# Optimization experiments

Hardware: AMD Instinct MI355X
Metric: run time of the kernel (lower is better)

## Reference

```python
import jax, jax.numpy as jnp
import numpy as np

TOP_K = 2


def setup_inputs() -> dict:
    key = jax.random.key(0)
    k1, k2, k3, k4, k5 = jax.random.split(key, 5)
    B, S, D, E, F = 2, 1024, 2048, 8, 768
    scale_in = 1.0 / np.sqrt(D)
    scale_ff = 1.0 / np.sqrt(F)
    return {
        "x": jax.random.normal(k1, (B, S, D), dtype=jnp.float32),
        "w_gate_router": jax.random.normal(k2, (E, D), dtype=jnp.float32) * scale_in,
        "w_gate_proj": jax.random.normal(k3, (E, F, D), dtype=jnp.float32) * scale_in,
        "w_up_proj": jax.random.normal(k4, (E, F, D), dtype=jnp.float32) * scale_in,
        "w_down_proj": jax.random.normal(k5, (E, D, F), dtype=jnp.float32) * scale_ff,
    }


def moe_forward(x, w_gate_router, w_gate_proj, w_up_proj, w_down_proj):
    E = w_gate_router.shape[0]
    # Router: scores [B,S,E], top-k selection, softmax over the k selected scores.
    scores = jnp.einsum("bsd,ed->bse", x, w_gate_router)
    topk_scores, topk_idx = jax.lax.top_k(scores, TOP_K)          # [B,S,K]
    topk_probs = jax.nn.softmax(topk_scores, axis=-1)             # [B,S,K]
    # Dense combine weights: zero for unselected experts (== scatter of topk_probs).
    weights = jnp.sum(topk_probs[..., None] * jax.nn.one_hot(topk_idx, E, dtype=x.dtype), axis=-2)  # [B,S,E]
    # Per-expert SwiGLU computed densely over all tokens (same math as
    # gather/dispatch-per-expert followed by scatter-add combine).
    gate = jnp.einsum("bsd,efd->bsef", x, w_gate_proj)            # [B,S,E,F]
    up = jnp.einsum("bsd,efd->bsef", x, w_up_proj)
    hidden = jax.nn.silu(gate) * up                                # [B,S,E,F]
    # Weighted combine: sum_e weights[b,s,e] * (hidden @ w_down[e].T)
    out = jnp.einsum("bsef,edf,bse->bsd", hidden, w_down_proj, weights)
    return out


def reference(x, w_gate_router, w_gate_proj, w_up_proj, w_down_proj):
    return moe_forward(x, w_gate_router, w_gate_proj, w_up_proj, w_down_proj)
```

## Files before the change

kernel.cpp:

```cpp
#include <hip/hip_runtime.h>

#define T_TOK 2048
#define DIM   2048
#define NEXP  8
#define FF    768
#define NGRP  16
#define BK    32

typedef unsigned short u16;
typedef unsigned int   u32;
typedef __bf16 bf16x8 __attribute__((ext_vector_type(8)));
typedef float  f32x4  __attribute__((ext_vector_type(4)));
typedef u16    u16x4  __attribute__((ext_vector_type(4)));
typedef u16    u16x8  __attribute__((ext_vector_type(8)));

#define AS1 __attribute__((address_space(1)))
#define AS3 __attribute__((address_space(3)))

__device__ __forceinline__ u16 f2bf(float f) {
    union { u32 i; float f; } v; v.f = f;
    u32 r = v.i + 0x7FFF + ((v.i >> 16) & 1);
    return (u16)(r >> 16);
}
__device__ __forceinline__ float bf2f(u16 u) {
    union { u32 i; float f; } v; v.i = ((u32)u) << 16; return v.f;
}

__device__ __forceinline__ void gload16(const u16* g, u16* l) {
    __builtin_amdgcn_global_load_lds((const AS1 u32*)g, (AS3 u32*)l, 16, 0, 0);
}

__global__ void cvt3_kernel(const float* __restrict__ s0, u16* __restrict__ d0,
                            const float* __restrict__ s1, u16* __restrict__ d1,
                            const float* __restrict__ s2, u16* __restrict__ d2) {
    const float* __restrict__ s; u16* __restrict__ d;
    switch (blockIdx.y) {
        case 0: s = s0; d = d0; break;
        case 1: s = s1; d = d1; break;
        default: s = s2; d = d2; break;
    }
    const size_t st = 1536u * 256u;
    size_t t = (size_t)blockIdx.x * 256 + threadIdx.x;
#pragma unroll
    for (int it = 0; it < 4; it++) {
        size_t i = t + (size_t)it * st;
        f32x4 a = ((const f32x4*)s)[i * 2];
        f32x4 b = ((const f32x4*)s)[i * 2 + 1];
        u16x8 o;
#pragma unroll
        for (int j = 0; j < 4; j++) { o[j] = f2bf(a[j]); o[4 + j] = f2bf(b[j]); }
        ((u16x8*)d)[i] = o;
    }
}

__global__ void router_kernel(const float* __restrict__ x, const float* __restrict__ wr,
                              int* cnt, int* rt_e, float* rt_p, u16* __restrict__ xb) {
    int wave = threadIdx.x >> 6, lane = threadIdx.x & 63;
    int t = blockIdx.x * 4 + wave;
    float xv[32];
#pragma unroll
    for (int i = 0; i < 32; i++) xv[i] = x[(size_t)t * DIM + i * 64 + lane];
#pragma unroll
    for (int i = 0; i < 32; i++) xb[(size_t)t * DIM + i * 64 + lane] = f2bf(xv[i]);
    float s[NEXP];
#pragma unroll
    for (int e = 0; e < NEXP; e++) {
        float acc = 0.f;
#pragma unroll
        for (int i = 0; i < 32; i++) acc += xv[i] * wr[(size_t)e * DIM + i * 64 + lane];
        for (int off = 32; off; off >>= 1) acc += __shfl_xor(acc, off);
        s[e] = acc;
    }
    if (lane == 0) {
        int bi = 0; float bv = s[0];
        for (int e = 1; e < NEXP; e++) if (s[e] > bv) { bv = s[e]; bi = e; }
        float sv = -1e30f; int si = 0;
        for (int e = 0; e < NEXP; e++) { if (e == bi) continue; if (s[e] > sv) { sv = s[e]; si = e; } }
        float p0 = 1.f / (1.f + __expf(sv - bv));
        float p1 = 1.f - p0;
        rt_e[t * 2 + 0] = bi; rt_e[t * 2 + 1] = si;
        rt_p[t * 2 + 0] = p0; rt_p[t * 2 + 1] = p1;
        atomicAdd(&cnt[bi * 2 + 0], 1);
        atomicAdd(&cnt[si * 2 + 1], 1);
    }
}

__global__ void scanassign_kernel(const int* cnt, const int* rt_e, const float* rt_p,
                                  int* base_g, int* tile_g, int* tile_m0, int* ntiles,
                                  int* rowtok, float* rowprob) {
    __shared__ int s_base[NGRP];
    __shared__ int s_pos[NGRP];
    int tid = threadIdx.x;
    if (tid < NGRP) s_pos[tid] = 0;
    if (tid < 64) {
        int lane = tid;
        int c = (lane < NGRP) ? cnt[lane] : 0;
        int nt_g = (c + 127) >> 7;
        int pre = 0, tpre = 0;
        for (int i = 0; i < NGRP; i++) {
            int ci = __shfl(c, i), ti = __shfl(nt_g, i);
            if (i < lane) { pre += ci; tpre += ti; }
        }
        if (lane < NGRP) {
            s_base[lane] = pre; base_g[lane] = pre;
            for (int j = 0; j < nt_g; j++) { tile_g[tpre + j] = lane; tile_m0[tpre + j] = j * 128; }
            if (lane == NGRP - 1) *ntiles = tpre + nt_g;
        }
    }
    __syncthreads();
    for (int t = tid; t < T_TOK; t += 256) {
#pragma unroll
        for (int k = 0; k < 2; k++) {
            int g = rt_e[t * 2 + k] * 2 + k;
            int pos = atomicAdd(&s_pos[g], 1);
            int row = s_base[g] + pos;
            rowtok[row] = t;
            rowprob[row] = rt_p[t * 2 + k];
        }
    }
}

__launch_bounds__(256)
__global__ void gateup_kernel(const u16* __restrict__ xb, const u16* __restrict__ wgb,
                              const u16* __restrict__ wub,
                              const int* cnt, const int* base, const int* tile_g,
                              const int* tile_m0, const int* ntiles,
                              const int* rowtok, const float* rowprob,
                              u16* __restrict__ hidden) {
    int tile = blockIdx.x;
    if (tile >= *ntiles) return;
    int g = tile_g[tile], m0 = tile_m0[tile];
    int e = g >> 1;
    int f0 = blockIdx.y * 32;
    int cg = cnt[g], bg_ = base[g];

    __shared__ u16 As[2][128 * BK];
    __shared__ u16 Bs[2][64 * BK];
    __shared__ int   tks[128];
    __shared__ float ps[128];

    int tid = threadIdx.x;
    if (tid < 128) {
        int valid = (m0 + tid) < cg;
        tks[tid] = valid ? rowtok[bg_ + m0 + tid] : 0;
        ps[tid]  = valid ? rowprob[bg_ + m0 + tid] : 0.f;
    }
    __syncthreads();

    int wave = tid >> 6, lane = tid & 63;
    int quad = lane >> 4, l16 = lane & 15;
    int wr = wave >> 1, wc = wave & 1;

    int r4 = lane >> 2;
    int cw = ((lane & 3) ^ ((r4 >> 1) & 3)) * 8;

    const u16* gA0 = xb + (size_t)tks[wave * 32 + r4] * DIM + cw;
    const u16* gA1 = xb + (size_t)tks[wave * 32 + 16 + r4] * DIM + cw;
    int lA0 = (wave * 32) * BK, lA1 = (wave * 32 + 16) * BK;
    const u16* bsrc = (wave & 1) ? wub : wgb;
    const u16* gB = bsrc + ((size_t)e * FF + f0 + (wave >> 1) * 16 + r4) * DIM + cw;
    int lB = (wave * 16) * BK;

    int swz = (quad ^ ((l16 >> 1) & 3)) * 8;
    int aoff[4], boff[2];
#pragma unroll
    for (int mi = 0; mi < 4; mi++) aoff[mi] = (wr * 64 + mi * 16 + l16) * BK + swz;
#pragma unroll
    for (int ni = 0; ni < 2; ni++) boff[ni] = (wc * 32 + ni * 16 + l16) * BK + swz;

    f32x4 acc[4][2] = {};

    gload16(gA0, &As[0][0] + lA0);
    gload16(gA1, &As[0][0] + lA1);
    gload16(gB,  &Bs[0][0] + lB);

    for (int kt = 0; kt < DIM / BK; kt++) {
        int cur = kt & 1;
        int kk = (kt + 1) * BK;
        if (kk < DIM) {
            gload16(gA0 + kk, &As[cur ^ 1][0] + lA0);
            gload16(gA1 + kk, &As[cur ^ 1][0] + lA1);
            gload16(gB + kk,  &Bs[cur ^ 1][0] + lB);
            __builtin_amdgcn_sched_barrier(0);
            asm volatile("s_waitcnt vmcnt(3)" ::: "memory");
        } else {
            __builtin_amdgcn_sched_barrier(0);
            asm volatile("s_waitcnt vmcnt(0)" ::: "memory");
        }
        __builtin_amdgcn_s_barrier();
        __builtin_amdgcn_sched_barrier(0);
        bf16x8 a[4], b[2];
#pragma unroll
        for (int mi = 0; mi < 4; mi++) a[mi] = *(const bf16x8*)&As[cur][aoff[mi]];
#pragma unroll
        for (int ni = 0; ni < 2; ni++) b[ni] = *(const bf16x8*)&Bs[cur][boff[ni]];
#pragma unroll
        for (int mi = 0; mi < 4; mi++)
#pragma unroll
            for (int ni = 0; ni < 2; ni++)
                acc[mi][ni] = __builtin_amdgcn_mfma_f32_16x16x32_bf16(a[mi], b[ni], acc[mi][ni], 0, 0, 0);
        __builtin_amdgcn_sched_barrier(0);
        asm volatile("s_waitcnt lgkmcnt(0)" ::: "memory");
        __builtin_amdgcn_s_barrier();
    }

    int f = f0 + wc * 16 + l16;
#pragma unroll
    for (int mi = 0; mi < 4; mi++) {
#pragma unroll
        for (int r = 0; r < 4; r++) {
            int m = wr * 64 + mi * 16 + quad * 4 + r;
            if (m0 + m < cg) {
                float gv = acc[mi][0][r], uv = acc[mi][1][r];
                float h = (gv / (1.f + __expf(-gv))) * uv * ps[m];
                hidden[(size_t)(bg_ + m0 + m) * FF + f] = f2bf(h);
            }
        }
    }
}

__launch_bounds__(256)
__global__ void down_kernel(const u16* __restrict__ hid, const u16* __restrict__ wdb,
                            const int* cnt, const int* base, const int* tile_g,
                            const int* tile_m0, const int* ntiles, const int* rowtok,
                            u16* __restrict__ out0, u16* __restrict__ out1) {
    int tile = blockIdx.x;
    if (tile >= *ntiles) return;
    int g = tile_g[tile], m0 = tile_m0[tile];
    int e = g >> 1, slot = g & 1;
    int d0 = blockIdx.y * 64;
    int cg = cnt[g], bg_ = base[g];

    __shared__ u16 As[2][128 * BK];
    __shared__ u16 Bs[2][64 * BK];
    __shared__ int tks[128];

    int tid = threadIdx.x;
    if (tid < 128) tks[tid] = ((m0 + tid) < cg) ? rowtok[bg_ + m0 + tid] : 0;
    __syncthreads();

    int wave = tid >> 6, lane = tid & 63;
    int quad = lane >> 4, l16 = lane & 15;
    int wr = wave >> 1, wc = wave & 1;

    int r4 = lane >> 2;
    int cw = ((lane & 3) ^ ((r4 >> 1) & 3)) * 8;

    const u16* gA0 = hid + (size_t)(bg_ + m0 + wave * 32 + r4) * FF + cw;
    const u16* gA1 = hid + (size_t)(bg_ + m0 + wave * 32 + 16 + r4) * FF + cw;
    int lA0 = (wave * 32) * BK, lA1 = (wave * 32 + 16) * BK;
    const u16* gB = wdb + ((size_t)e * DIM + d0 + wave * 16 + r4) * FF + cw;
    int lB = (wave * 16) * BK;

    int swz = (quad ^ ((l16 >> 1) & 3)) * 8;
    int aoff[4], boff[2];
#pragma unroll
    for (int mi = 0; mi < 4; mi++) aoff[mi] = (wr * 64 + mi * 16 + l16) * BK + swz;
#pragma unroll
    for (int ni = 0; ni < 2; ni++) boff[ni] = (wc * 32 + ni * 16 + l16) * BK + swz;

    f32x4 acc[4][2] = {};

    gload16(gA0, &As[0][0] + lA0);
    gload16(gA1, &As[0][0] + lA1);
    gload16(gB,  &Bs[0][0] + lB);

    for (int kt = 0; kt < FF / BK; kt++) {
        int cur = kt & 1;
        int kk = (kt + 1) * BK;
        if (kk < FF) {
            gload16(gA0 + kk, &As[cur ^ 1][0] + lA0);
            gload16(gA1 + kk, &As[cur ^ 1][0] + lA1);
            gload16(gB + kk,  &Bs[cur ^ 1][0] + lB);
            __builtin_amdgcn_sched_barrier(0);
            asm volatile("s_waitcnt vmcnt(3)" ::: "memory");
        } else {
            __builtin_amdgcn_sched_barrier(0);
            asm volatile("s_waitcnt vmcnt(0)" ::: "memory");
        }
        __builtin_amdgcn_s_barrier();
        __builtin_amdgcn_sched_barrier(0);
        bf16x8 a[4], b[2];
#pragma unroll
        for (int mi = 0; mi < 4; mi++) a[mi] = *(const bf16x8*)&As[cur][aoff[mi]];
#pragma unroll
        for (int ni = 0; ni < 2; ni++) b[ni] = *(const bf16x8*)&Bs[cur][boff[ni]];
#pragma unroll
        for (int mi = 0; mi < 4; mi++)
#pragma unroll
            for (int ni = 0; ni < 2; ni++)
                acc[mi][ni] = __builtin_amdgcn_mfma_f32_16x16x32_bf16(a[mi], b[ni], acc[mi][ni], 0, 0, 0);
        __builtin_amdgcn_sched_barrier(0);
        asm volatile("s_waitcnt lgkmcnt(0)" ::: "memory");
        __builtin_amdgcn_s_barrier();
    }

    u16* outp = slot ? out1 : out0;
#pragma unroll
    for (int mi = 0; mi < 4; mi++) {
#pragma unroll
        for (int ni = 0; ni < 2; ni++) {
            int d = d0 + wc * 32 + ni * 16 + l16;
#pragma unroll
            for (int r = 0; r < 4; r++) {
                int m = wr * 64 + mi * 16 + quad * 4 + r;
                if (m0 + m < cg) {
                    outp[(size_t)tks[m] * DIM + d] = f2bf(acc[mi][ni][r]);
                }
            }
        }
    }
}

__global__ void combine_kernel(const u16* __restrict__ o0, const u16* __restrict__ o1,
                               float* __restrict__ out) {
    int i = blockIdx.x * blockDim.x + threadIdx.x;
    u16x8 a = *(const u16x8*)(o0 + (size_t)i * 8);
    u16x8 b = *(const u16x8*)(o1 + (size_t)i * 8);
    f32x4 r0, r1;
#pragma unroll
    for (int j = 0; j < 4; j++) {
        r0[j] = bf2f(a[j]) + bf2f(b[j]);
        r1[j] = bf2f(a[4 + j]) + bf2f(b[4 + j]);
    }
    *(f32x4*)(out + (size_t)i * 8) = r0;
    *(f32x4*)(out + (size_t)i * 8 + 4) = r1;
}

extern "C" void kernel_launch(void* const* d_in, const int* in_sizes, int n_in,
                              void* d_out, int out_size, void* d_ws, size_t ws_size,
                              hipStream_t stream) {
    const float* x  = (const float*)d_in[0];
    const float* wr = (const float*)d_in[1];
    const float* wg = (const float*)d_in[2];
    const float* wu = (const float*)d_in[3];
    const float* wd = (const float*)d_in[4];
    float* out = (float*)d_out;

    char* W = (char*)d_ws;
    int*   cnt     = (int*)(W + 0);
    int*   base    = (int*)(W + 128);
    int*   ntiles  = (int*)(W + 192);
    int*   tile_g  = (int*)(W + 256);
    int*   tile_m0 = (int*)(W + 512);
    int*   rt_e    = (int*)(W + 1024);
    float* rt_p    = (float*)(W + 20480);
    int*   rowtok  = (int*)(W + 40960);
    float* rowprob = (float*)(W + 61440);
    u16*   hidden  = (u16*)(W + 81920);
    u16*   xb      = (u16*)(W + ((size_t)8  << 20));
    u16*   wgb     = (u16*)(W + ((size_t)17 << 20));
    u16*   wub     = (u16*)(W + ((size_t)43 << 20));
    u16*   wdb     = (u16*)(W + ((size_t)69 << 20));
    u16*   out0    = (u16*)(W + ((size_t)17 << 20));
    u16*   out1    = (u16*)(W + ((size_t)26 << 20));

    hipMemsetAsync(W, 0, 256, stream);

    cvt3_kernel<<<dim3(1536, 3), 256, 0, stream>>>(wg, wgb, wu, wub, wd, wdb);

    router_kernel<<<T_TOK / 4, 256, 0, stream>>>(x, wr, cnt, rt_e, rt_p, xb);
    scanassign_kernel<<<1, 256, 0, stream>>>(cnt, rt_e, rt_p, base, tile_g, tile_m0,
                                             ntiles, rowtok, rowprob);

    gateup_kernel<<<dim3(48, 24), 256, 0, stream>>>(xb, wgb, wub, cnt, base, tile_g, tile_m0,
                                                    ntiles, rowtok, rowprob, hidden);
    down_kernel<<<dim3(48, 32), 256, 0, stream>>>(hidden, wdb, cnt, base, tile_g, tile_m0,
                                                  ntiles, rowtok, out0, out1);
    combine_kernel<<<T_TOK * DIM / (256 * 8), 256, 0, stream>>>(out0, out1, out);
}
```

Baseline: 381.2 us.

## Deepen gate-up and down GEMM pipelines to three LDS stages with BK=64

Both the grouped gate/up GEMM and the down GEMM now use a K tile of 64 instead of 32, with a triple-buffered LDS ring that keeps two tiles of global-to-LDS loads in flight. The XOR swizzle is reworked for 8-element column groups so the wider rows stay bank-conflict free. This halves the number of K iterations and their barriers and hides more load latency. In exchange LDS use per block roughly triples (about 72KB), which may cut occupancy, and the hard-coded vmcnt wait counts must match the number of loads issued per stage.

```diff
diff --git a/kernel.cpp b/kernel.cpp
--- a/kernel.cpp
+++ b/kernel.cpp
@@ -5,7 +5,7 @@
 #define NEXP  8
 #define FF    768
 #define NGRP  16
-#define BK    32
+#define BK    64
 
 typedef unsigned short u16;
 typedef unsigned int   u32;
@@ -134,8 +134,8 @@
     int f0 = blockIdx.y * 32;
     int cg = cnt[g], bg_ = base[g];
 
-    __shared__ u16 As[2][128 * BK];
-    __shared__ u16 Bs[2][64 * BK];
+    __shared__ u16 As[3][128 * BK];
+    __shared__ u16 Bs[3][64 * BK];
     __shared__ int   tks[128];
     __shared__ float ps[128];
 
@@ -151,58 +151,88 @@
     int quad = lane >> 4, l16 = lane & 15;
     int wr = wave >> 1, wc = wave & 1;
 
-    int r4 = lane >> 2;
-    int cw = ((lane & 3) ^ ((r4 >> 1) & 3)) * 8;
-
-    const u16* gA0 = xb + (size_t)tks[wave * 32 + r4] * DIM + cw;
-    const u16* gA1 = xb + (size_t)tks[wave * 32 + 16 + r4] * DIM + cw;
-    int lA0 = (wave * 32) * BK, lA1 = (wave * 32 + 16) * BK;
+    int r8  = lane >> 3;
+    int csw = ((lane & 7) ^ r8) * 8;
+
+    const u16* gA[4]; int lA[4];
+#pragma unroll
+    for (int gi = 0; gi < 4; gi++) {
+        int row = wave * 32 + gi * 8 + r8;
+        gA[gi] = xb + (size_t)tks[row] * DIM + csw;
+        lA[gi] = (wave * 32 + gi * 8) * BK;
+    }
     const u16* bsrc = (wave & 1) ? wub : wgb;
-    const u16* gB = bsrc + ((size_t)e * FF + f0 + (wave >> 1) * 16 + r4) * DIM + cw;
-    int lB = (wave * 16) * BK;
-
-    int swz = (quad ^ ((l16 >> 1) & 3)) * 8;
-    int aoff[4], boff[2];
-#pragma unroll
-    for (int mi = 0; mi < 4; mi++) aoff[mi] = (wr * 64 + mi * 16 + l16) * BK + swz;
-#pragma unroll
-    for (int ni = 0; ni < 2; ni++) boff[ni] = (wc * 32 + ni * 16 + l16) * BK + swz;
+    const u16* gB[2]; int lB[2];
+#pragma unroll
+    for (int gi = 0; gi < 2; gi++) {
+        int f = f0 + (wave >> 1) * 16 + gi * 8 + r8;
+        gB[gi] = bsrc + ((size_t)e * FF + f) * DIM + csw;
+        lB[gi] = (wave * 16 + gi * 8) * BK;
+    }
+
+    int sw0 = ((0 * 4 + quad) ^ (l16 & 7)) * 8;
+    int sw1 = ((1 * 4 + quad) ^ (l16 & 7)) * 8;
 
     f32x4 acc[4][2] = {};
 
-    gload16(gA0, &As[0][0] + lA0);
-    gload16(gA1, &As[0][0] + lA1);
-    gload16(gB,  &Bs[0][0] + lB);
-
-    for (int kt = 0; kt < DIM / BK; kt++) {
-        int cur = kt & 1;
-        int kk = (kt + 1) * BK;
-        if (kk < DIM) {
-            gload16(gA0 + kk, &As[cur ^ 1][0] + lA0);
-            gload16(gA1 + kk, &As[cur ^ 1][0] + lA1);
-            gload16(gB + kk,  &Bs[cur ^ 1][0] + lB);
-            __builtin_amdgcn_sched_barrier(0);
-            asm volatile("s_waitcnt vmcnt(3)" ::: "memory");
-        } else {
-            __builtin_amdgcn_sched_barrier(0);
-            asm volatile("s_waitcnt vmcnt(0)" ::: "memory");
-        }
+#define GU_STAGE(kkof, bi) do {                                          \
+    _Pragma("unroll")                                                    \
+    for (int gi = 0; gi < 4; gi++) gload16(gA[gi] + (kkof), &As[bi][0] + lA[gi]); \
+    _Pragma("unroll")                                                    \
+    for (int gi = 0; gi < 2; gi++) gload16(gB[gi] + (kkof), &Bs[bi][0] + lB[gi]); \
+} while (0)
+
+#define GU_COMPUTE(bi) do {                                              \
+    _Pragma("unroll")                                                    \
+    for (int ks = 0; ks < 2; ks++) {                                     \
+        int sw = ks ? sw1 : sw0;                                         \
+        bf16x8 a[4], b[2];                                               \
+        _Pragma("unroll")                                                \
+        for (int mi = 0; mi < 4; mi++)                                   \
+            a[mi] = *(const bf16x8*)&As[bi][(wr * 64 + mi * 16 + l16) * BK + sw]; \
+        _Pragma("unroll")                                                \
+        for (int ni = 0; ni < 2; ni++)                                   \
+            b[ni] = *(const bf16x8*)&Bs[bi][(wc * 32 + ni * 16 + l16) * BK + sw]; \
+        _Pragma("unroll")                                                \
+        for (int mi = 0; mi < 4; mi++)                                   \
+            _Pragma("unroll")                                            \
+            for (int ni = 0; ni < 2; ni++)                               \
+                acc[mi][ni] = __builtin_amdgcn_mfma_f32_16x16x32_bf16(a[mi], b[ni], acc[mi][ni], 0, 0, 0); \
+    }                                                                    \
+} while (0)
+
+    GU_STAGE(0, 0);
+    GU_STAGE(BK, 1);
+
+    const int NT = DIM / BK;
+    int cur = 0;
+    for (int kt = 0; kt < NT - 2; kt++) {
+        int s2 = cur + 2; if (s2 >= 3) s2 -= 3;
+        GU_STAGE((kt + 2) * BK, s2);
+        __builtin_amdgcn_sched_barrier(0);
+        asm volatile("s_waitcnt vmcnt(12)" ::: "memory");
         __builtin_amdgcn_s_barrier();
         __builtin_amdgcn_sched_barrier(0);
-        bf16x8 a[4], b[2];
-#pragma unroll
-        for (int mi = 0; mi < 4; mi++) a[mi] = *(const bf16x8*)&As[cur][aoff[mi]];
-#pragma unroll
-        for (int ni = 0; ni < 2; ni++) b[ni] = *(const bf16x8*)&Bs[cur][boff[ni]];
-#pragma unroll
-        for (int mi = 0; mi < 4; mi++)
-#pragma unroll
-            for (int ni = 0; ni < 2; ni++)
-                acc[mi][ni] = __builtin_amdgcn_mfma_f32_16x16x32_bf16(a[mi], b[ni], acc[mi][ni], 0, 0, 0);
+        GU_COMPUTE(cur);
         __builtin_amdgcn_sched_barrier(0);
         asm volatile("s_waitcnt lgkmcnt(0)" ::: "memory");
         __builtin_amdgcn_s_barrier();
-    }
+        cur++; if (cur >= 3) cur = 0;
+    }
+    __builtin_amdgcn_sched_barrier(0);
+    asm volatile("s_waitcnt vmcnt(6)" ::: "memory");
+    __builtin_amdgcn_s_barrier();
+    __builtin_amdgcn_sched_barrier(0);
+    GU_COMPUTE(cur);
+    cur++; if (cur >= 3) cur = 0;
+    __builtin_amdgcn_sched_barrier(0);
+    asm volatile("s_waitcnt vmcnt(0)" ::: "memory");
+    __builtin_amdgcn_s_barrier();
+    __builtin_amdgcn_sched_barrier(0);
+    GU_COMPUTE(cur);
+
+#undef GU_STAGE
+#undef GU_COMPUTE
 
     int f = f0 + wc * 16 + l16;
 #pragma unroll
@@ -231,8 +261,8 @@
     int d0 = blockIdx.y * 64;
     int cg = cnt[g], bg_ = base[g];
 
-    __shared__ u16 As[2][128 * BK];
-    __shared__ u16 Bs[2][64 * BK];
+    __shared__ u16 As[3][128 * BK];
+    __shared__ u16 Bs[3][64 * BK];
     __shared__ int tks[128];
 
     int tid = threadIdx.x;
@@ -243,57 +273,87 @@
     int quad = lane >> 4, l16 = lane & 15;
     int wr = wave >> 1, wc = wave & 1;
 
-    int r4 = lane >> 2;
-    int cw = ((lane & 3) ^ ((r4 >> 1) & 3)) * 8;
-
-    const u16* gA0 = hid + (size_t)(bg_ + m0 + wave * 32 + r4) * FF + cw;
-    const u16* gA1 = hid + (size_t)(bg_ + m0 + wave * 32 + 16 + r4) * FF + cw;
-    int lA0 = (wave * 32) * BK, lA1 = (wave * 32 + 16) * BK;
-    const u16* gB = wdb + ((size_t)e * DIM + d0 + wave * 16 + r4) * FF + cw;
-    int lB = (wave * 16) * BK;
-
-    int swz = (quad ^ ((l16 >> 1) & 3)) * 8;
-    int aoff[4], boff[2];
-#pragma unroll
-    for (int mi = 0; mi < 4; mi++) aoff[mi] = (wr * 64 + mi * 16 + l16) * BK + swz;
-#pragma unroll
-    for (int ni = 0; ni < 2; ni++) boff[ni] = (wc * 32 + ni * 16 + l16) * BK + swz;
+    int r8  = lane >> 3;
+    int csw = ((lane & 7) ^ r8) * 8;
+
+    const u16* gA[4]; int lA[4];
+#pragma unroll
+    for (int gi = 0; gi < 4; gi++) {
+        int row = wave * 32 + gi * 8 + r8;
+        gA[gi] = hid + (size_t)(bg_ + m0 + row) * FF + csw;
+        lA[gi] = (wave * 32 + gi * 8) * BK;
+    }
+    const u16* gB[2]; int lB[2];
+#pragma unroll
+    for (int gi = 0; gi < 2; gi++) {
+        int n = wave * 16 + gi * 8 + r8;
+        gB[gi] = wdb + ((size_t)e * DIM + d0 + n) * FF + csw;
+        lB[gi] = (wave * 16 + gi * 8) * BK;
+    }
+
+    int sw0 = ((0 * 4 + quad) ^ (l16 & 7)) * 8;
+    int sw1 = ((1 * 4 + quad) ^ (l16 & 7)) * 8;
 
     f32x4 acc[4][2] = {};
 
-    gload16(gA0, &As[0][0] + lA0);
-    gload16(gA1, &As[0][0] + lA1);
-    gload16(gB,  &Bs[0][0] + lB);
-
-    for (int kt = 0; kt < FF / BK; kt++) {
-        int cur = kt & 1;
-        int kk = (kt + 1) * BK;
-        if (kk < FF) {
-            gload16(gA0 + kk, &As[cur ^ 1][0] + lA0);
-            gload16(gA1 + kk, &As[cur ^ 1][0] + lA1);
-            gload16(gB + kk,  &Bs[cur ^ 1][0] + lB);
-            __builtin_amdgcn_sched_barrier(0);
-            asm volatile("s_waitcnt vmcnt(3)" ::: "memory");
-        } else {
-            __builtin_amdgcn_sched_barrier(0);
-            asm volatile("s_waitcnt vmcnt(0)" ::: "memory");
-        }
+#define DN_STAGE(kkof, bi) do {                                          \
+    _Pragma("unroll")                                                    \
+    for (int gi = 0; gi < 4; gi++) gload16(gA[gi] + (kkof), &As[bi][0] + lA[gi]); \
+    _Pragma("unroll")                                                    \
+    for (int gi = 0; gi < 2; gi++) gload16(gB[gi] + (kkof), &Bs[bi][0] + lB[gi]); \
+} while (0)
+
+#define DN_COMPUTE(bi) do {                                              \
+    _Pragma("unroll")                                                    \
+    for (int ks = 0; ks < 2; ks++) {                                     \
+        int sw = ks ? sw1 : sw0;                                         \
+        bf16x8 a[4], b[2];                                               \
+        _Pragma("unroll")                                                \
+        for (int mi = 0; mi < 4; mi++)                                   \
+            a[mi] = *(const bf16x8*)&As[bi][(wr * 64 + mi * 16 + l16) * BK + sw]; \
+        _Pragma("unroll")                                                \
+        for (int ni = 0; ni < 2; ni++)                                   \
+            b[ni] = *(const bf16x8*)&Bs[bi][(wc * 32 + ni * 16 + l16) * BK + sw]; \
+        _Pragma("unroll")                                                \
+        for (int mi = 0; mi < 4; mi++)                                   \
+            _Pragma("unroll")                                            \
+            for (int ni = 0; ni < 2; ni++)                               \
+                acc[mi][ni] = __builtin_amdgcn_mfma_f32_16x16x32_bf16(a[mi], b[ni], acc[mi][ni], 0, 0, 0); \
+    }                                                                    \
+} while (0)
+
+    DN_STAGE(0, 0);
+    DN_STAGE(BK, 1);
+
+    const int NT = FF / BK;
+    int cur = 0;
+    for (int kt = 0; kt < NT - 2; kt++) {
+        int s2 = cur + 2; if (s2 >= 3) s2 -= 3;
+        DN_STAGE((kt + 2) * BK, s2);
+        __builtin_amdgcn_sched_barrier(0);
+        asm volatile("s_waitcnt vmcnt(12)" ::: "memory");
         __builtin_amdgcn_s_barrier();
         __builtin_amdgcn_sched_barrier(0);
-        bf16x8 a[4], b[2];
-#pragma unroll
-        for (int mi = 0; mi < 4; mi++) a[mi] = *(const bf16x8*)&As[cur][aoff[mi]];
-#pragma unroll
-        for (int ni = 0; ni < 2; ni++) b[ni] = *(const bf16x8*)&Bs[cur][boff[ni]];
-#pragma unroll
-        for (int mi = 0; mi < 4; mi++)
-#pragma unroll
-            for (int ni = 0; ni < 2; ni++)
-                acc[mi][ni] = __builtin_amdgcn_mfma_f32_16x16x32_bf16(a[mi], b[ni], acc[mi][ni], 0, 0, 0);
+        DN_COMPUTE(cur);
         __builtin_amdgcn_sched_barrier(0);
         asm volatile("s_waitcnt lgkmcnt(0)" ::: "memory");
         __builtin_amdgcn_s_barrier();
-    }
+        cur++; if (cur >= 3) cur = 0;
+    }
+    __builtin_amdgcn_sched_barrier(0);
+    asm volatile("s_waitcnt vmcnt(6)" ::: "memory");
+    __builtin_amdgcn_s_barrier();
+    __builtin_amdgcn_sched_barrier(0);
+    DN_COMPUTE(cur);
+    cur++; if (cur >= 3) cur = 0;
+    __builtin_amdgcn_sched_barrier(0);
+    asm volatile("s_waitcnt vmcnt(0)" ::: "memory");
+    __builtin_amdgcn_s_barrier();
+    __builtin_amdgcn_sched_barrier(0);
+    DN_COMPUTE(cur);
+
+#undef DN_STAGE
+#undef DN_COMPUTE
 
     u16* outp = slot ? out1 : out0;
 #pragma unroll
```

After: 378.5 us. Within noise of the previous version (-0.7%).
